# Kernel optimization log

Measured on AMD Instinct MI355X. Metric: run time of the kernel, lower is better.

The kernel has to match this reference:

```python
import jax, jax.numpy as jnp
import numpy as np

N_NODES = 100000
N_EDGES = 1000000
IN_CH, HID_CH, N_CLS = 128, 64, 40


def setup_inputs() -> dict:
    key = jax.random.key(0)
    ks = jax.random.split(key, 8)
    x = jax.random.normal(ks[0], (N_NODES, IN_CH), dtype=jnp.float32)
    edge_index = jax.random.randint(ks[1], (2, N_EDGES), 0, N_NODES, dtype=jnp.int32)
    # Glorot-ish scaled weights (ARMAConv init_weight / root_weight, K=1 stack squeezed)
    w1_init = jax.random.normal(ks[2], (IN_CH, HID_CH), dtype=jnp.float32) / np.sqrt(IN_CH)
    w1_root = jax.random.normal(ks[3], (IN_CH, HID_CH), dtype=jnp.float32) / np.sqrt(IN_CH)
    b1 = jnp.zeros((HID_CH,), dtype=jnp.float32)
    w2_init = jax.random.normal(ks[4], (HID_CH, N_CLS), dtype=jnp.float32) / np.sqrt(HID_CH)
    w2_root = jax.random.normal(ks[5], (HID_CH, N_CLS), dtype=jnp.float32) / np.sqrt(HID_CH)
    b2 = jnp.zeros((N_CLS,), dtype=jnp.float32)
    return {"x": x, "edge_index": edge_index,
            "w1_init": w1_init, "w1_root": w1_root, "b1": b1,
            "w2_init": w2_init, "w2_root": w2_root, "b2": b2}


def _arma_layer(x, row, col, norm, w_init, w_root, bias):
    # ARMAConv, num_stacks=1, num_layers=1, shared_weights=True, eval mode (dropout=id):
    # out = relu( A_hat @ (x W_init) + x W_root + b ), mean over the single stack.
    h = x @ w_init                           # [N, F_out]
    msg = norm[:, None] * h[row]             # gather from source nodes, [E, F_out]
    agg = jax.ops.segment_sum(msg, col, num_segments=N_NODES)  # scatter-add at targets
    return jax.nn.relu(agg + x @ w_root + bias)


def reference(x, edge_index, w1_init, w1_root, b1, w2_init, w2_root, b2):
    row, col = edge_index[0], edge_index[1]
    # gcn_norm, add_self_loops=False: deg over targets, norm = d^-1/2[row] * d^-1/2[col]
    deg = jax.ops.segment_sum(jnp.ones((row.shape[0],), x.dtype), col, num_segments=N_NODES)
    dinv = jnp.where(deg > 0, jax.lax.rsqrt(jnp.maximum(deg, 1e-12)), jnp.zeros_like(deg))
    norm = dinv[row] * dinv[col]
    h = _arma_layer(x, row, col, norm, w1_init, w1_root, b1)
    h = jax.nn.relu(h)  # BiARMA relu; dropout identity in eval
    return _arma_layer(h, row, col, norm, w2_init, w2_root, b2)
```

## Files before the change

kernel.cpp:

```cpp
#include <hip/hip_runtime.h>

#define N_NODES 100000
#define N_EDGES 1000000
#define IN_CH 128
#define HID_CH 64
#define N_CLS 40

#define NBUCK 782

static inline int cdiv(int a, int b) { return (a + b - 1) / b; }

using bf16x8 = __attribute__((ext_vector_type(8))) short;
using f32x4  = __attribute__((ext_vector_type(4))) float;

__device__ __forceinline__ unsigned pack_bf2(float a, float b) {
    unsigned ua = __float_as_uint(a), ub = __float_as_uint(b);
    ua += 0x7fffu + ((ua >> 16) & 1u);
    ub += 0x7fffu + ((ub >> 16) & 1u);
    return (ua >> 16) | (ub & 0xffff0000u);
}
__device__ __forceinline__ unsigned short bf16_of(float a) {
    unsigned ua = __float_as_uint(a);
    ua += 0x7fffu + ((ua >> 16) & 1u);
    return (unsigned short)(ua >> 16);
}
__device__ __forceinline__ float bf_lo(unsigned u) { return __uint_as_float(u << 16); }
__device__ __forceinline__ float bf_hi(unsigned u) { return __uint_as_float(u & 0xffff0000u); }


__global__ __launch_bounds__(256)
void bucket_count_kernel(const int* __restrict__ cols, int* __restrict__ gcount, int E) {
    __shared__ int hist[NBUCK];
    for (int i = threadIdx.x; i < NBUCK; i += 256) hist[i] = 0;
    __syncthreads();
    int per = (E + gridDim.x - 1) / gridDim.x;
    int s = blockIdx.x * per;
    int e = min(E, s + per);
    for (int j = s + threadIdx.x; j < e; j += 256)
        atomicAdd(&hist[cols[j] >> 7], 1);
    __syncthreads();
    for (int i = threadIdx.x; i < NBUCK; i += 256)
        if (hist[i]) atomicAdd(&gcount[i], hist[i]);
}


__global__ __launch_bounds__(1024)
void scan_bucket_kernel(const int* __restrict__ gcount, int* __restrict__ boff,
                        int* __restrict__ gcursor, int* __restrict__ offsets) {
    __shared__ int part[1024];
    int t = threadIdx.x;
    part[t] = (t < NBUCK) ? gcount[t] : 0;
    __syncthreads();
    for (int off = 1; off < 1024; off <<= 1) {
        int v = (t >= off) ? part[t - off] : 0;
        __syncthreads();
        part[t] += v;
        __syncthreads();
    }
    int excl = (t > 0) ? part[t - 1] : 0;
    if (t < NBUCK) { boff[t] = excl; gcursor[t] = excl; }
    if (t == NBUCK) { boff[NBUCK] = excl; offsets[N_NODES] = excl; }
}


__global__ __launch_bounds__(256)
void bucket_scatter_kernel(const int* __restrict__ rows, const int* __restrict__ cols,
                           int* __restrict__ gcursor, int* __restrict__ pedge, int E) {
    __shared__ int cur[NBUCK];
    for (int i = threadIdx.x; i < NBUCK; i += 256) cur[i] = 0;
    __syncthreads();
    int per = (E + gridDim.x - 1) / gridDim.x;
    int s = blockIdx.x * per;
    int e = min(E, s + per);
    for (int j = s + threadIdx.x; j < e; j += 256)
        atomicAdd(&cur[cols[j] >> 7], 1);
    __syncthreads();
    for (int i = threadIdx.x; i < NBUCK; i += 256) {
        int h = cur[i];
        cur[i] = h ? atomicAdd(&gcursor[i], h) : 0;
    }
    __syncthreads();
    for (int j = s + threadIdx.x; j < e; j += 256) {
        int c = cols[j];
        int pos = atomicAdd(&cur[c >> 7], 1);
        pedge[pos] = (rows[j] << 7) | (c & 127);
    }
}


__global__ __launch_bounds__(256)
void bucket_sort_kernel(const int* __restrict__ boff, const int* __restrict__ pedge,
                        int* __restrict__ srow, int* __restrict__ offsets,
                        float* __restrict__ dinv) {
    __shared__ int cnt[128];
    __shared__ int scn[128];
    __shared__ int cur[128];
    int b = blockIdx.x, t = threadIdx.x;
    if (t < 128) cnt[t] = 0;
    __syncthreads();
    int e0 = boff[b], e1 = boff[b + 1];
    for (int j = e0 + t; j < e1; j += 256)
        atomicAdd(&cnt[pedge[j] & 127], 1);
    __syncthreads();
    if (t < 128) scn[t] = cnt[t];
    __syncthreads();
    for (int off = 1; off < 128; off <<= 1) {
        int v = 0;
        if (t < 128 && t >= off) v = scn[t - off];
        __syncthreads();
        if (t < 128) scn[t] += v;
        __syncthreads();
    }
    if (t < 128) {
        int excl = (t > 0) ? scn[t - 1] : 0;
        cur[t] = excl;
        int node = b * 128 + t;
        if (node < N_NODES) {
            offsets[node] = e0 + excl;
            dinv[node] = cnt[t] ? rsqrtf((float)cnt[t]) : 0.f;
        }
    }
    __syncthreads();
    for (int j = e0 + t; j < e1; j += 256) {
        int p = pedge[j];
        int pos = atomicAdd(&cur[p & 127], 1);
        srow[e0 + pos] = p >> 7;
    }
}


template<int K, int C1, int C2>
__launch_bounds__(256)
__global__ void gemm_mfma_fused_kernel(const float* __restrict__ X,
                                       const float* __restrict__ W1,
                                       const float* __restrict__ W2,
                                       const float* __restrict__ Bias,
                                       const float* __restrict__ dinv,
                                       unsigned short* __restrict__ Y1b,
                                       float* __restrict__ Y2, int N) {
    constexpr int CT = C1 + C2;
    constexpr int NT = CT / 16;
    constexpr int KS = K / 32;
    constexpr int KP = (K + 8) / 2;
    static_assert(CT % 16 == 0 && K % 32 == 0, "shape");
    static_assert(C1 % 4 == 0 && C2 % 4 == 0, "staging vec4");

    __shared__ unsigned xb[64 * KP];
    __shared__ unsigned wt[CT * KP];
    __shared__ float dloc[64];

    const int tid = threadIdx.x;
    const int wave = tid >> 6;
    const int lane = tid & 63;
    const int m = lane & 15;
    const int quad = lane >> 4;
    const int r0 = blockIdx.x * 64;

    if (tid < 64) {
        int gr = r0 + tid;
        dloc[tid] = (gr < N) ? dinv[gr] : 0.f;
    }

    constexpr int XIT = 64 * (K / 4);
    for (int i = tid; i < XIT; i += 256) {
        int rr = i / (K / 4);
        int k4 = i - rr * (K / 4);
        int gr = r0 + rr;
        float4 v = make_float4(0.f, 0.f, 0.f, 0.f);
        if (gr < N)
            v = *reinterpret_cast<const float4*>(&X[(size_t)gr * K + k4 * 4]);
        uint2 p;
        p.x = pack_bf2(v.x, v.y);
        p.y = pack_bf2(v.z, v.w);
        *reinterpret_cast<uint2*>(&xb[rr * KP + k4 * 2]) = p;
    }

    constexpr int WIT = (K / 2) * (CT / 4);
    for (int i = tid; i < WIT; i += 256) {
        int kp = i / (CT / 4);
        int c4 = i - kp * (CT / 4);
        int k = kp * 2;
        int c = c4 * 4;
        float4 va, vb;
        if (c < C1) {
            va = *reinterpret_cast<const float4*>(&W1[(size_t)k * C1 + c]);
            vb = *reinterpret_cast<const float4*>(&W1[(size_t)(k + 1) * C1 + c]);
        } else {
            va = *reinterpret_cast<const float4*>(&W2[(size_t)k * C2 + (c - C1)]);
            vb = *reinterpret_cast<const float4*>(&W2[(size_t)(k + 1) * C2 + (c - C1)]);
        }
        wt[(c + 0) * KP + kp] = pack_bf2(va.x, vb.x);
        wt[(c + 1) * KP + kp] = pack_bf2(va.y, vb.y);
        wt[(c + 2) * KP + kp] = pack_bf2(va.z, vb.z);
        wt[(c + 3) * KP + kp] = pack_bf2(va.w, vb.w);
    }
    __syncthreads();

    const int rowbase = wave * 16;
    f32x4 acc[NT];
#pragma unroll
    for (int t = 0; t < NT; ++t) acc[t] = (f32x4){0.f, 0.f, 0.f, 0.f};

#pragma unroll
    for (int ks = 0; ks < KS; ++ks) {
        bf16x8 a = *reinterpret_cast<const bf16x8*>(&xb[(rowbase + m) * KP + ks * 16 + quad * 4]);
#pragma unroll
        for (int t = 0; t < NT; ++t) {
            bf16x8 b = *reinterpret_cast<const bf16x8*>(&wt[(t * 16 + m) * KP + ks * 16 + quad * 4]);
            acc[t] = __builtin_amdgcn_mfma_f32_16x16x32_bf16(a, b, acc[t], 0, 0, 0);
        }
    }

#pragma unroll
    for (int t = 0; t < NT; ++t) {
        int c = t * 16 + m;
        float bias = (c >= C1) ? Bias[c - C1] : 0.f;
#pragma unroll
        for (int reg = 0; reg < 4; ++reg) {
            int rl = rowbase + quad * 4 + reg;
            int r = r0 + rl;
            if (r >= N) continue;
            float v = acc[t][reg];
            if (c < C1) {
                Y1b[(size_t)r * C1 + c] = bf16_of(v * dloc[rl]);
            } else {
                Y2[(size_t)r * C2 + (c - C1)] = v + bias;
            }
        }
    }
}


template<int C>
__launch_bounds__(256)
__global__ void pull_bf16_kernel(const int* __restrict__ offsets,
                                 const int* __restrict__ srow,
                                 const float* __restrict__ dinv,
                                 const unsigned* __restrict__ H,
                                 float* __restrict__ Y, int N) {
    constexpr int TPE = C / 4;
    constexpr int CH = C / 2;
    int gid = blockIdx.x * blockDim.x + threadIdx.x;
    int node = gid / TPE;
    int lane = gid - node * TPE;
    if (node >= N) return;

    int e0 = offsets[node];
    int e1 = offsets[node + 1];
    float dc = dinv[node];

    float4 acc = make_float4(0.f, 0.f, 0.f, 0.f);
    int j = e0;
    for (; j + 4 <= e1; j += 4) {
        int r0 = srow[j + 0];
        int r1 = srow[j + 1];
        int r2 = srow[j + 2];
        int r3 = srow[j + 3];
        uint2 u0 = *reinterpret_cast<const uint2*>(&H[(size_t)r0 * CH + lane * 2]);
        uint2 u1 = *reinterpret_cast<const uint2*>(&H[(size_t)r1 * CH + lane * 2]);
        uint2 u2 = *reinterpret_cast<const uint2*>(&H[(size_t)r2 * CH + lane * 2]);
        uint2 u3 = *reinterpret_cast<const uint2*>(&H[(size_t)r3 * CH + lane * 2]);
        acc.x += (bf_lo(u0.x) + bf_lo(u1.x)) + (bf_lo(u2.x) + bf_lo(u3.x));
        acc.y += (bf_hi(u0.x) + bf_hi(u1.x)) + (bf_hi(u2.x) + bf_hi(u3.x));
        acc.z += (bf_lo(u0.y) + bf_lo(u1.y)) + (bf_lo(u2.y) + bf_lo(u3.y));
        acc.w += (bf_hi(u0.y) + bf_hi(u1.y)) + (bf_hi(u2.y) + bf_hi(u3.y));
    }
    for (; j < e1; ++j) {
        int r = srow[j];
        uint2 u = *reinterpret_cast<const uint2*>(&H[(size_t)r * CH + lane * 2]);
        acc.x += bf_lo(u.x);
        acc.y += bf_hi(u.x);
        acc.z += bf_lo(u.y);
        acc.w += bf_hi(u.y);
    }

    float4* Y4 = reinterpret_cast<float4*>(Y);
    size_t yi = (size_t)node * TPE + lane;
    float4 y = Y4[yi];
    y.x = fmaxf(fmaf(dc, acc.x, y.x), 0.f);
    y.y = fmaxf(fmaf(dc, acc.y, y.y), 0.f);
    y.z = fmaxf(fmaf(dc, acc.z, y.z), 0.f);
    y.w = fmaxf(fmaf(dc, acc.w, y.w), 0.f);
    Y4[yi] = y;
}


extern "C" void kernel_launch(void* const* d_in, const int* in_sizes, int n_in,
                              void* d_out, int out_size, void* d_ws, size_t ws_size,
                              hipStream_t stream) {
    const float* x       = (const float*)d_in[0];
    const int*   eidx    = (const int*)d_in[1];
    const float* w1_init = (const float*)d_in[2];
    const float* w1_root = (const float*)d_in[3];
    const float* b1      = (const float*)d_in[4];
    const float* w2_init = (const float*)d_in[5];
    const float* w2_root = (const float*)d_in[6];
    const float* b2      = (const float*)d_in[7];
    float* out = (float*)d_out;

    const int* rows = eidx;
    const int* cols = eidx + N_EDGES;

    int* wsi = (int*)d_ws;
    int*      gcount  = wsi;
    int*      boff    = wsi + 784;
    int*      gcursor = wsi + 1572;
    float*    dinv    = (float*)(wsi + 2360);
    int*      offsets = wsi + 102360;
    int*      srow    = wsi + 202364;
    unsigned* h0b     = (unsigned*)(wsi + 1202364);
    int*      pedge   = wsi + 1202364;
    float*    agg1    = (float*)(wsi + 4402364);
    unsigned* h2b     = h0b;

    hipMemsetAsync(gcount, 0, 784 * sizeof(int), stream);
    bucket_count_kernel<<<128, 256, 0, stream>>>(cols, gcount, N_EDGES);
    scan_bucket_kernel<<<1, 1024, 0, stream>>>(gcount, boff, gcursor, offsets);
    bucket_scatter_kernel<<<128, 256, 0, stream>>>(rows, cols, gcursor, pedge, N_EDGES);
    bucket_sort_kernel<<<NBUCK, 256, 0, stream>>>(boff, pedge, srow, offsets, dinv);

    const int GGRID = cdiv(N_NODES, 64);

    gemm_mfma_fused_kernel<IN_CH, HID_CH, HID_CH><<<GGRID, 256, 0, stream>>>(
        x, w1_init, w1_root, b1, dinv, (unsigned short*)h0b, agg1, N_NODES);
    pull_bf16_kernel<HID_CH><<<cdiv(N_NODES * (HID_CH / 4), 256), 256, 0, stream>>>(
        offsets, srow, dinv, h0b, agg1, N_NODES);

    gemm_mfma_fused_kernel<HID_CH, N_CLS, N_CLS><<<GGRID, 256, 0, stream>>>(
        agg1, w2_init, w2_root, b2, dinv, (unsigned short*)h2b, out, N_NODES);
    pull_bf16_kernel<N_CLS><<<cdiv(N_NODES * (N_CLS / 4), 256), 256, 0, stream>>>(
        offsets, srow, dinv, h2b, out, N_NODES);
}
```

Before: 264.5 us.

## Pre-pack bf16 weights once and feed MFMA directly from global memory

Adds a small kernel that converts and transposes both layers' weights into bf16 pairs once per call. The GEMM kernels drop their LDS staging and barrier: each lane loads its X row fragment straight from global memory, converts it to bf16 in registers, and reads pre-packed weight fragments from global (L2-cached) memory. This removes per-block repeated weight conversion and LDS traffic, at the cost of an extra launch and uncoalesced-ish global loads for B fragments.

```diff
diff --git a/kernel.cpp b/kernel.cpp
--- a/kernel.cpp
+++ b/kernel.cpp
@@ -129,100 +129,94 @@
 }
 
 
+__global__ __launch_bounds__(256)
+void pack_w_kernel(const float* __restrict__ W1i, const float* __restrict__ W1r,
+                   const float* __restrict__ W2i, const float* __restrict__ W2r,
+                   unsigned* __restrict__ wt1, unsigned* __restrict__ wt2) {
+    int i = blockIdx.x * 256 + threadIdx.x;
+    if (i < 128 * 64) {
+        int c = i >> 6, kp = i & 63;
+        int k = kp * 2;
+        float a, b;
+        if (c < 64) { a = W1i[k * 64 + c];        b = W1i[(k + 1) * 64 + c]; }
+        else        { a = W1r[k * 64 + (c - 64)]; b = W1r[(k + 1) * 64 + (c - 64)]; }
+        wt1[i] = pack_bf2(a, b);
+    } else {
+        int j = i - 128 * 64;
+        if (j < 80 * 32) {
+            int c = j >> 5, kp = j & 31;
+            int k = kp * 2;
+            float a, b;
+            if (c < 40) { a = W2i[k * 40 + c];        b = W2i[(k + 1) * 40 + c]; }
+            else        { a = W2r[k * 40 + (c - 40)]; b = W2r[(k + 1) * 40 + (c - 40)]; }
+            wt2[j] = pack_bf2(a, b);
+        }
+    }
+}
+
+
 template<int K, int C1, int C2>
 __launch_bounds__(256)
-__global__ void gemm_mfma_fused_kernel(const float* __restrict__ X,
-                                       const float* __restrict__ W1,
-                                       const float* __restrict__ W2,
-                                       const float* __restrict__ Bias,
-                                       const float* __restrict__ dinv,
-                                       unsigned short* __restrict__ Y1b,
-                                       float* __restrict__ Y2, int N) {
+__global__ void gemm_mfma_direct_kernel(const float* __restrict__ X,
+                                        const unsigned* __restrict__ WTG,
+                                        const float* __restrict__ Bias,
+                                        const float* __restrict__ dinv,
+                                        unsigned short* __restrict__ Y1b,
+                                        float* __restrict__ Y2, int N) {
     constexpr int CT = C1 + C2;
     constexpr int NT = CT / 16;
     constexpr int KS = K / 32;
-    constexpr int KP = (K + 8) / 2;
+    constexpr int KPI = K / 2;
     static_assert(CT % 16 == 0 && K % 32 == 0, "shape");
-    static_assert(C1 % 4 == 0 && C2 % 4 == 0, "staging vec4");
-
-    __shared__ unsigned xb[64 * KP];
-    __shared__ unsigned wt[CT * KP];
-    __shared__ float dloc[64];
 
     const int tid = threadIdx.x;
     const int wave = tid >> 6;
     const int lane = tid & 63;
     const int m = lane & 15;
     const int quad = lane >> 4;
-    const int r0 = blockIdx.x * 64;
-
-    if (tid < 64) {
-        int gr = r0 + tid;
-        dloc[tid] = (gr < N) ? dinv[gr] : 0.f;
-    }
-
-    constexpr int XIT = 64 * (K / 4);
-    for (int i = tid; i < XIT; i += 256) {
-        int rr = i / (K / 4);
-        int k4 = i - rr * (K / 4);
-        int gr = r0 + rr;
-        float4 v = make_float4(0.f, 0.f, 0.f, 0.f);
-        if (gr < N)
-            v = *reinterpret_cast<const float4*>(&X[(size_t)gr * K + k4 * 4]);
-        uint2 p;
-        p.x = pack_bf2(v.x, v.y);
-        p.y = pack_bf2(v.z, v.w);
-        *reinterpret_cast<uint2*>(&xb[rr * KP + k4 * 2]) = p;
-    }
-
-    constexpr int WIT = (K / 2) * (CT / 4);
-    for (int i = tid; i < WIT; i += 256) {
-        int kp = i / (CT / 4);
-        int c4 = i - kp * (CT / 4);
-        int k = kp * 2;
-        int c = c4 * 4;
-        float4 va, vb;
-        if (c < C1) {
-            va = *reinterpret_cast<const float4*>(&W1[(size_t)k * C1 + c]);
-            vb = *reinterpret_cast<const float4*>(&W1[(size_t)(k + 1) * C1 + c]);
-        } else {
-            va = *reinterpret_cast<const float4*>(&W2[(size_t)k * C2 + (c - C1)]);
-            vb = *reinterpret_cast<const float4*>(&W2[(size_t)(k + 1) * C2 + (c - C1)]);
+    const int r0 = blockIdx.x * 64 + wave * 16;
+
+    int arow = r0 + m;
+    const float* xrow = X + (size_t)(arow < N ? arow : 0) * K;
+
+    f32x4 acc[NT];
+#pragma unroll
+    for (int t = 0; t < NT; ++t) acc[t] = (f32x4){0.f, 0.f, 0.f, 0.f};
+
+#pragma unroll
+    for (int ks = 0; ks < KS; ++ks) {
+        const float* xp = xrow + ks * 32 + quad * 8;
+        float4 v0 = *reinterpret_cast<const float4*>(xp);
+        float4 v1 = *reinterpret_cast<const float4*>(xp + 4);
+        union { unsigned u[4]; bf16x8 v; } A;
+        A.u[0] = pack_bf2(v0.x, v0.y);
+        A.u[1] = pack_bf2(v0.z, v0.w);
+        A.u[2] = pack_bf2(v1.x, v1.y);
+        A.u[3] = pack_bf2(v1.z, v1.w);
+#pragma unroll
+        for (int t = 0; t < NT; ++t) {
+            bf16x8 b = *reinterpret_cast<const bf16x8*>(&WTG[(t * 16 + m) * KPI + ks * 16 + quad * 4]);
+            acc[t] = __builtin_amdgcn_mfma_f32_16x16x32_bf16(A.v, b, acc[t], 0, 0, 0);
         }
-        wt[(c + 0) * KP + kp] = pack_bf2(va.x, vb.x);
-        wt[(c + 1) * KP + kp] = pack_bf2(va.y, vb.y);
-        wt[(c + 2) * KP + kp] = pack_bf2(va.z, vb.z);
-        wt[(c + 3) * KP + kp] = pack_bf2(va.w, vb.w);
-    }
-    __syncthreads();
-
-    const int rowbase = wave * 16;
-    f32x4 acc[NT];
-#pragma unroll
-    for (int t = 0; t < NT; ++t) acc[t] = (f32x4){0.f, 0.f, 0.f, 0.f};
-
-#pragma unroll
-    for (int ks = 0; ks < KS; ++ks) {
-        bf16x8 a = *reinterpret_cast<const bf16x8*>(&xb[(rowbase + m) * KP + ks * 16 + quad * 4]);
-#pragma unroll
-        for (int t = 0; t < NT; ++t) {
-            bf16x8 b = *reinterpret_cast<const bf16x8*>(&wt[(t * 16 + m) * KP + ks * 16 + quad * 4]);
-            acc[t] = __builtin_amdgcn_mfma_f32_16x16x32_bf16(a, b, acc[t], 0, 0, 0);
-        }
-    }
-
+    }
+
+    float dr[4];
+#pragma unroll
+    for (int reg = 0; reg < 4; ++reg) {
+        int r = r0 + quad * 4 + reg;
+        dr[reg] = (r < N) ? dinv[r] : 0.f;
+    }
 #pragma unroll
     for (int t = 0; t < NT; ++t) {
         int c = t * 16 + m;
         float bias = (c >= C1) ? Bias[c - C1] : 0.f;
 #pragma unroll
         for (int reg = 0; reg < 4; ++reg) {
-            int rl = rowbase + quad * 4 + reg;
-            int r = r0 + rl;
+            int r = r0 + quad * 4 + reg;
             if (r >= N) continue;
             float v = acc[t][reg];
             if (c < C1) {
-                Y1b[(size_t)r * C1 + c] = bf16_of(v * dloc[rl]);
+                Y1b[(size_t)r * C1 + c] = bf16_of(v * dr[reg]);
             } else {
                 Y2[(size_t)r * C2 + (c - C1)] = v + bias;
             }
@@ -305,15 +299,19 @@
     int*      gcount  = wsi;
     int*      boff    = wsi + 784;
     int*      gcursor = wsi + 1572;
-    float*    dinv    = (float*)(wsi + 2360);
-    int*      offsets = wsi + 102360;
-    int*      srow    = wsi + 202364;
-    unsigned* h0b     = (unsigned*)(wsi + 1202364);
-    int*      pedge   = wsi + 1202364;
-    float*    agg1    = (float*)(wsi + 4402364);
+    unsigned* wt1g    = (unsigned*)(wsi + 2360);
+    unsigned* wt2g    = (unsigned*)(wsi + 10552);
+    float*    dinv    = (float*)(wsi + 13112);
+    int*      offsets = wsi + 113112;
+    int*      srow    = wsi + 213116;
+    unsigned* h0b     = (unsigned*)(wsi + 1213116);
+    int*      pedge   = wsi + 1213116;
+    float*    agg1    = (float*)(wsi + 4413116);
     unsigned* h2b     = h0b;
 
     hipMemsetAsync(gcount, 0, 784 * sizeof(int), stream);
+    pack_w_kernel<<<cdiv(128 * 64 + 80 * 32, 256), 256, 0, stream>>>(
+        w1_init, w1_root, w2_init, w2_root, wt1g, wt2g);
     bucket_count_kernel<<<128, 256, 0, stream>>>(cols, gcount, N_EDGES);
     scan_bucket_kernel<<<1, 1024, 0, stream>>>(gcount, boff, gcursor, offsets);
     bucket_scatter_kernel<<<128, 256, 0, stream>>>(rows, cols, gcursor, pedge, N_EDGES);
@@ -321,13 +319,13 @@
 
     const int GGRID = cdiv(N_NODES, 64);
 
-    gemm_mfma_fused_kernel<IN_CH, HID_CH, HID_CH><<<GGRID, 256, 0, stream>>>(
-        x, w1_init, w1_root, b1, dinv, (unsigned short*)h0b, agg1, N_NODES);
+    gemm_mfma_direct_kernel<IN_CH, HID_CH, HID_CH><<<GGRID, 256, 0, stream>>>(
+        x, wt1g, b1, dinv, (unsigned short*)h0b, agg1, N_NODES);
     pull_bf16_kernel<HID_CH><<<cdiv(N_NODES * (HID_CH / 4), 256), 256, 0, stream>>>(
         offsets, srow, dinv, h0b, agg1, N_NODES);
 
-    gemm_mfma_fused_kernel<HID_CH, N_CLS, N_CLS><<<GGRID, 256, 0, stream>>>(
-        agg1, w2_init, w2_root, b2, dinv, (unsigned short*)h2b, out, N_NODES);
+    gemm_mfma_direct_kernel<HID_CH, N_CLS, N_CLS><<<GGRID, 256, 0, stream>>>(
+        agg1, wt2g, b2, dinv, (unsigned short*)h2b, out, N_NODES);
     pull_bf16_kernel<N_CLS><<<cdiv(N_NODES * (N_CLS / 4), 256), 256, 0, stream>>>(
         offsets, srow, dinv, h2b, out, N_NODES);
 }
```

New measurement: 273.3 us. +3.3%, slower.
